# Performance work log

Measured on AMD Instinct MI355X. Metric: run time of the kernel, lower is better.

The kernel has to match this reference:

```python
import jax, jax.numpy as jnp
import numpy as np
from jax import lax

INPUT, HIDDEN, OUT = 5, 32, 2

def setup_inputs() -> dict:
    key = jax.random.key(0)
    ks = jax.random.split(key, 7)
    s_ih = 1.0 / np.sqrt(HIDDEN)
    return {
        "x": jax.random.normal(ks[0], (16384, 200, INPUT), dtype=jnp.float32),
        "W_ih": jax.random.uniform(ks[1], (4 * HIDDEN, INPUT), jnp.float32, -s_ih, s_ih),
        "W_hh": jax.random.uniform(ks[2], (4 * HIDDEN, HIDDEN), jnp.float32, -s_ih, s_ih),
        "b_ih": jax.random.uniform(ks[3], (4 * HIDDEN,), jnp.float32, -s_ih, s_ih),
        "b_hh": jax.random.uniform(ks[4], (4 * HIDDEN,), jnp.float32, -s_ih, s_ih),
        "W_fc": jax.random.uniform(ks[5], (OUT, HIDDEN), jnp.float32, -s_ih, s_ih),
        "b_fc": jax.random.uniform(ks[6], (OUT,), jnp.float32, -s_ih, s_ih),
    }

def reference(x, W_ih, W_hh, b_ih, b_hh, W_fc, b_fc):
    B = x.shape[0]
    # Precompute input projections for all timesteps in one GEMM: [B,T,4H]
    x_proj = jnp.einsum("bti,gi->btg", x, W_ih) + (b_ih + b_hh)
    xs = jnp.swapaxes(x_proj, 0, 1)  # [T, B, 4H]

    def step(carry, xg):
        h, c = carry
        gates = xg + h @ W_hh.T  # [B, 4H]
        i, f, g, o = jnp.split(gates, 4, axis=-1)  # torch gate order i,f,g,o
        i = jax.nn.sigmoid(i)
        f = jax.nn.sigmoid(f)
        g = jnp.tanh(g)
        o = jax.nn.sigmoid(o)
        c = f * c + i * g
        h = o * jnp.tanh(c)
        return (h, c), None

    h0 = jnp.zeros((B, HIDDEN), x.dtype)
    c0 = jnp.zeros((B, HIDDEN), x.dtype)
    (h_n, _), _ = lax.scan(step, (h0, c0), xs)
    return h_n @ W_fc.T + b_fc  # [B, 2]
```

## Files before the change

### kernel.cpp

```cpp
#include <hip/hip_runtime.h>


typedef __bf16 bf16x8 __attribute__((ext_vector_type(8)));
typedef float  f32x4  __attribute__((ext_vector_type(4)));
typedef unsigned int u32;

constexpr int kT = 200, kIN = 5, kH = 32;
constexpr int CT   = 40;
constexpr int HSTR = 40;

union FragU { bf16x8 v; __bf16 b[8]; unsigned short s[8]; u32 u[4]; uint4 q4; };

__device__ __forceinline__ unsigned short bfbits(__bf16 b) {
    union { __bf16 b; unsigned short s; } u; u.b = b; return u.s;
}
__device__ __forceinline__ void split2(float x, __bf16& hi, __bf16& lo) {
    hi = (__bf16)x;
    lo = (__bf16)(x - (float)hi);
}
__device__ __forceinline__ float sigm(float z) {
    return __builtin_amdgcn_rcpf(1.0f + __builtin_amdgcn_exp2f(-1.4426950408889634f * z));
}
__device__ __forceinline__ float tanhv(float z) {
    return fmaf(2.0f,
        __builtin_amdgcn_rcpf(1.0f + __builtin_amdgcn_exp2f(-2.8853900817779268f * z)),
        -1.0f);
}

__global__ __launch_bounds__(128) void lstm_mfma2(
    const float* __restrict__ x,
    const float* __restrict__ W_ih,
    const float* __restrict__ W_hh,
    const float* __restrict__ b_ih,
    const float* __restrict__ b_hh,
    const float* __restrict__ W_fc,
    const float* __restrict__ b_fc,
    float* __restrict__ out)
{
    __shared__ uint4 xbuf[CT][33];
    __shared__ __align__(16) __bf16 hbh[2][16 * HSTR];
    __shared__ __align__(16) __bf16 hbl[2][16 * HSTR];

    const int tid  = threadIdx.x;
    const int wv   = tid >> 6;
    const int lane = tid & 63;
    const int n16  = lane & 15;
    const int q    = lane >> 4;
    const int b0   = blockIdx.x * 16;

    bf16x8 whhh[4], whhl[4], wihf[4];
#pragma unroll
    for (int g = 0; g < 4; ++g) {
        const int t = 2 * g + wv;
        const int r = t * 16 + n16;
        FragU H, L;
#pragma unroll
        for (int j = 0; j < 8; ++j)
            split2(W_hh[r * kH + q * 8 + j], H.b[j], L.b[j]);
        whhh[g] = H.v; whhl[g] = L.v;

        float wr[5];
#pragma unroll
        for (int i = 0; i < 5; ++i) wr[i] = W_ih[r * kIN + i];
        __bf16 bh, bl;
        split2(b_ih[r] + b_hh[r], bh, bl);

        FragU F;
        F.u[0] = F.u[1] = F.u[2] = F.u[3] = 0u;
        if (q == 0) {
#pragma unroll
            for (int i = 0; i < 5; ++i) F.b[i] = (__bf16)wr[i];
#pragma unroll
            for (int i = 0; i < 3; ++i) F.b[5 + i] = (__bf16)wr[i];
        } else if (q == 1) {
            F.b[0] = (__bf16)wr[3];
            F.b[1] = (__bf16)wr[4];
#pragma unroll
            for (int i = 0; i < 5; ++i) {
                __bf16 hb, lb; split2(wr[i], hb, lb);
                F.b[2 + i] = lb;
            }
            F.b[7] = bh;
        } else if (q == 2) {
            F.b[0] = bl;
        }
        wihf[g] = F.v;
    }

    {
        u32* z0 = (u32*)&hbh[0][0];
        u32* z1 = (u32*)&hbl[0][0];
        for (int i = tid; i < (16 * HSTR) / 2; i += 128) { z0[i] = 0u; z1[i] = 0u; }
    }

    float cst[4] = {0.f, 0.f, 0.f, 0.f};

    const int hro = n16 * HSTR + q * 8;
    const int hwo = (q * 4) * HSTR + n16 + 16 * wv;

    auto step = [&](int tc, const __bf16* sh, const __bf16* sl,
                    __bf16* dh, __bf16* dl) {
        FragU xf;
        if (q < 2) {
            xf.q4 = xbuf[tc][n16 * 2 + q];
        } else if (q == 2) {
            xf.u[0] = 0x3F80u; xf.u[1] = 0u; xf.u[2] = 0u; xf.u[3] = 0u;
        } else {
            xf.u[0] = 0u; xf.u[1] = 0u; xf.u[2] = 0u; xf.u[3] = 0u;
        }

        bf16x8 AH = *(const bf16x8*)(sh + hro);
        bf16x8 AL = *(const bf16x8*)(sl + hro);

        f32x4 acc[4];
#pragma unroll
        for (int g = 0; g < 4; ++g) {
            f32x4 a = {0.f, 0.f, 0.f, 0.f};
            a = __builtin_amdgcn_mfma_f32_16x16x32_bf16(xf.v, wihf[g], a, 0, 0, 0);
            a = __builtin_amdgcn_mfma_f32_16x16x32_bf16(AH,   whhh[g], a, 0, 0, 0);
            a = __builtin_amdgcn_mfma_f32_16x16x32_bf16(AH,   whhl[g], a, 0, 0, 0);
            a = __builtin_amdgcn_mfma_f32_16x16x32_bf16(AL,   whhh[g], a, 0, 0, 0);
            acc[g] = a;
        }

#pragma unroll
        for (int r = 0; r < 4; ++r) {
            float iv = sigm (acc[0][r]);
            float fv = sigm (acc[1][r]);
            float gv = tanhv(acc[2][r]);
            float ov = sigm (acc[3][r]);
            float cn = fmaf(fv, cst[r], iv * gv);
            cst[r] = cn;
            float hn = ov * tanhv(cn);
            __bf16 hh, hl;
            split2(hn, hh, hl);
            dh[hwo + r * HSTR] = hh;
            dl[hwo + r * HSTR] = hl;
        }
        __syncthreads();
    };

    for (int phase = 0; phase < kT / CT; ++phase) {
        {
            const int mm = tid >> 3, pp = tid & 7;
            const float* xrow = x + (size_t)(b0 + mm) * (kT * kIN)
                                  + (size_t)(phase * CT + pp * 5) * kIN;
            float xv[25];
#pragma unroll
            for (int i = 0; i < 25; ++i) xv[i] = xrow[i];
#pragma unroll
            for (int s5 = 0; s5 < 5; ++s5) {
                u32 xh[5], xl[5];
#pragma unroll
                for (int i = 0; i < 5; ++i) {
                    __bf16 hb, lb; split2(xv[s5 * 5 + i], hb, lb);
                    xh[i] = bfbits(hb); xl[i] = bfbits(lb);
                }
                uint4 f0 = make_uint4(xh[0] | (xh[1] << 16),
                                      xh[2] | (xh[3] << 16),
                                      xh[4] | (xl[0] << 16),
                                      xl[1] | (xl[2] << 16));
                uint4 f1 = make_uint4(xl[3] | (xl[4] << 16),
                                      xh[0] | (xh[1] << 16),
                                      xh[2] | (xh[3] << 16),
                                      xh[4] | (0x3F80u << 16));
                const int tc = pp * 5 + s5;
                xbuf[tc][mm * 2 + 0] = f0;
                xbuf[tc][mm * 2 + 1] = f1;
            }
        }
        __syncthreads();

#pragma unroll 1
        for (int tc = 0; tc < CT; tc += 2) {
            step(tc,     hbh[0], hbl[0], hbh[1], hbl[1]);
            step(tc + 1, hbh[1], hbl[1], hbh[0], hbl[0]);
        }
    }

    if (tid < 32) {
        const int m = tid >> 1, o = tid & 1;
        float s = b_fc[o];
#pragma unroll
        for (int j = 0; j < kH; ++j) {
            float hv = (float)hbh[0][m * HSTR + j] + (float)hbl[0][m * HSTR + j];
            s = fmaf(hv, W_fc[o * kH + j], s);
        }
        out[(size_t)(b0 + m) * 2 + o] = s;
    }
}

extern "C" void kernel_launch(void* const* d_in, const int* in_sizes, int n_in,
                              void* d_out, int out_size, void* d_ws, size_t ws_size,
                              hipStream_t stream) {
    const float* x    = (const float*)d_in[0];
    const float* W_ih = (const float*)d_in[1];
    const float* W_hh = (const float*)d_in[2];
    const float* b_ih = (const float*)d_in[3];
    const float* b_hh = (const float*)d_in[4];
    const float* W_fc = (const float*)d_in[5];
    const float* b_fc = (const float*)d_in[6];
    float* out = (float*)d_out;

    hipLaunchKernelGGL(lstm_mfma2, dim3(1024), dim3(128), 0, stream,
                       x, W_ih, W_hh, b_ih, b_hh, W_fc, b_fc, out);
}
```

Measured before the change: 283.7 us.

## Keep LSTM hidden state in registers with single-wave transposed MFMA recurrence

Replaces the two-wave block, which exchanged h through shared memory with a barrier every timestep, with a single 64-lane wave. The weights are used as the A operand so each lane's MFMA output rows line up with the B-fragment layout, and h stays in registers across steps. The input projection for the next timestep is issued early as separate MFMAs, overlapping it with the gate math, and the per-step __syncthreads and LDS round trip go away. In exchange each wave now does twice the MFMA and transcendental work, and occupancy halves per block while register pressure rises.

```diff
diff --git a/kernel.cpp b/kernel.cpp
--- a/kernel.cpp
+++ b/kernel.cpp
@@ -6,8 +6,7 @@
 typedef unsigned int u32;
 
 constexpr int kT = 200, kIN = 5, kH = 32;
-constexpr int CT   = 40;
-constexpr int HSTR = 40;
+constexpr int CT = 40;
 
 union FragU { bf16x8 v; __bf16 b[8]; unsigned short s[8]; u32 u[4]; uint4 q4; };
 
@@ -27,7 +26,7 @@
         -1.0f);
 }
 
-__global__ __launch_bounds__(128) void lstm_mfma2(
+__global__ __launch_bounds__(64) void lstm_reg(
     const float* __restrict__ x,
     const float* __restrict__ W_ih,
     const float* __restrict__ W_hh,
@@ -37,33 +36,29 @@
     const float* __restrict__ b_fc,
     float* __restrict__ out)
 {
-    __shared__ uint4 xbuf[CT][33];
-    __shared__ __align__(16) __bf16 hbh[2][16 * HSTR];
-    __shared__ __align__(16) __bf16 hbl[2][16 * HSTR];
-
-    const int tid  = threadIdx.x;
-    const int wv   = tid >> 6;
-    const int lane = tid & 63;
+    __shared__ uint4 xbuf[CT][34];
+
+    const int lane = threadIdx.x;
     const int n16  = lane & 15;
     const int q    = lane >> 4;
     const int b0   = blockIdx.x * 16;
 
-    bf16x8 whhh[4], whhl[4], wihf[4];
-#pragma unroll
-    for (int g = 0; g < 4; ++g) {
-        const int t = 2 * g + wv;
-        const int r = t * 16 + n16;
+    bf16x8 whhA_h[8], whhA_l[8], wihA[8];
+#pragma unroll
+    for (int t8 = 0; t8 < 8; ++t8) {
+        const int g  = t8 & 3, hb = t8 >> 2;
+        const int R  = g * 32 + 8 * (n16 >> 2) + 4 * hb + (n16 & 3);
         FragU H, L;
 #pragma unroll
         for (int j = 0; j < 8; ++j)
-            split2(W_hh[r * kH + q * 8 + j], H.b[j], L.b[j]);
-        whhh[g] = H.v; whhl[g] = L.v;
+            split2(W_hh[R * kH + q * 8 + j], H.b[j], L.b[j]);
+        whhA_h[t8] = H.v; whhA_l[t8] = L.v;
 
         float wr[5];
 #pragma unroll
-        for (int i = 0; i < 5; ++i) wr[i] = W_ih[r * kIN + i];
+        for (int i = 0; i < 5; ++i) wr[i] = W_ih[R * kIN + i];
         __bf16 bh, bl;
-        split2(b_ih[r] + b_hh[r], bh, bl);
+        split2(b_ih[R] + b_hh[R], bh, bl);
 
         FragU F;
         F.u[0] = F.u[1] = F.u[2] = F.u[3] = 0u;
@@ -77,84 +72,50 @@
             F.b[1] = (__bf16)wr[4];
 #pragma unroll
             for (int i = 0; i < 5; ++i) {
-                __bf16 hb, lb; split2(wr[i], hb, lb);
-                F.b[2 + i] = lb;
+                __bf16 hbb, lbb; split2(wr[i], hbb, lbb);
+                F.b[2 + i] = lbb;
             }
             F.b[7] = bh;
         } else if (q == 2) {
             F.b[0] = bl;
         }
-        wihf[g] = F.v;
-    }
-
-    {
-        u32* z0 = (u32*)&hbh[0][0];
-        u32* z1 = (u32*)&hbl[0][0];
-        for (int i = tid; i < (16 * HSTR) / 2; i += 128) { z0[i] = 0u; z1[i] = 0u; }
-    }
-
-    float cst[4] = {0.f, 0.f, 0.f, 0.f};
-
-    const int hro = n16 * HSTR + q * 8;
-    const int hwo = (q * 4) * HSTR + n16 + 16 * wv;
-
-    auto step = [&](int tc, const __bf16* sh, const __bf16* sl,
-                    __bf16* dh, __bf16* dl) {
-        FragU xf;
-        if (q < 2) {
-            xf.q4 = xbuf[tc][n16 * 2 + q];
-        } else if (q == 2) {
-            xf.u[0] = 0x3F80u; xf.u[1] = 0u; xf.u[2] = 0u; xf.u[3] = 0u;
-        } else {
-            xf.u[0] = 0u; xf.u[1] = 0u; xf.u[2] = 0u; xf.u[3] = 0u;
-        }
-
-        bf16x8 AH = *(const bf16x8*)(sh + hro);
-        bf16x8 AL = *(const bf16x8*)(sl + hro);
-
-        f32x4 acc[4];
-#pragma unroll
-        for (int g = 0; g < 4; ++g) {
-            f32x4 a = {0.f, 0.f, 0.f, 0.f};
-            a = __builtin_amdgcn_mfma_f32_16x16x32_bf16(xf.v, wihf[g], a, 0, 0, 0);
-            a = __builtin_amdgcn_mfma_f32_16x16x32_bf16(AH,   whhh[g], a, 0, 0, 0);
-            a = __builtin_amdgcn_mfma_f32_16x16x32_bf16(AH,   whhl[g], a, 0, 0, 0);
-            a = __builtin_amdgcn_mfma_f32_16x16x32_bf16(AL,   whhh[g], a, 0, 0, 0);
-            acc[g] = a;
-        }
-
-#pragma unroll
-        for (int r = 0; r < 4; ++r) {
-            float iv = sigm (acc[0][r]);
-            float fv = sigm (acc[1][r]);
-            float gv = tanhv(acc[2][r]);
-            float ov = sigm (acc[3][r]);
-            float cn = fmaf(fv, cst[r], iv * gv);
-            cst[r] = cn;
-            float hn = ov * tanhv(cn);
-            __bf16 hh, hl;
-            split2(hn, hh, hl);
-            dh[hwo + r * HSTR] = hh;
-            dl[hwo + r * HSTR] = hl;
-        }
-        __syncthreads();
-    };
+        wihA[t8] = F.v;
+    }
+
+    for (int t2 = lane; t2 < CT; t2 += 64) {
+        xbuf[t2][32] = make_uint4(0x3F80u, 0u, 0u, 0u);
+        xbuf[t2][33] = make_uint4(0u, 0u, 0u, 0u);
+    }
+
+    const int col = (q < 2) ? (n16 * 2 + q) : (30 + q);
+    const f32x4 zf4 = {0.f, 0.f, 0.f, 0.f};
+
+    float c8[8] = {0.f, 0.f, 0.f, 0.f, 0.f, 0.f, 0.f, 0.f};
+    float hf[8] = {0.f, 0.f, 0.f, 0.f, 0.f, 0.f, 0.f, 0.f};
+    FragU Bh, Bl;
+    Bh.u[0] = Bh.u[1] = Bh.u[2] = Bh.u[3] = 0u;
+    Bl.u[0] = Bl.u[1] = Bl.u[2] = Bl.u[3] = 0u;
+
+    f32x4 xn[8];
 
     for (int phase = 0; phase < kT / CT; ++phase) {
         {
-            const int mm = tid >> 3, pp = tid & 7;
-            const float* xrow = x + (size_t)(b0 + mm) * (kT * kIN)
-                                  + (size_t)(phase * CT + pp * 5) * kIN;
-            float xv[25];
-#pragma unroll
-            for (int i = 0; i < 25; ++i) xv[i] = xrow[i];
-#pragma unroll
-            for (int s5 = 0; s5 < 5; ++s5) {
+            const int mm = lane >> 2, pp = lane & 3;
+            const float2* xr2 = (const float2*)(x + (size_t)(b0 + mm) * (kT * kIN)
+                                                  + (size_t)(phase * CT + pp * 10) * kIN);
+            float xv[50];
+#pragma unroll
+            for (int i = 0; i < 25; ++i) {
+                float2 v = xr2[i];
+                xv[2 * i] = v.x; xv[2 * i + 1] = v.y;
+            }
+#pragma unroll
+            for (int s5 = 0; s5 < 10; ++s5) {
                 u32 xh[5], xl[5];
 #pragma unroll
                 for (int i = 0; i < 5; ++i) {
-                    __bf16 hb, lb; split2(xv[s5 * 5 + i], hb, lb);
-                    xh[i] = bfbits(hb); xl[i] = bfbits(lb);
+                    __bf16 hbb, lbb; split2(xv[s5 * 5 + i], hbb, lbb);
+                    xh[i] = bfbits(hbb); xl[i] = bfbits(lbb);
                 }
                 uint4 f0 = make_uint4(xh[0] | (xh[1] << 16),
                                       xh[2] | (xh[3] << 16),
@@ -164,28 +125,67 @@
                                       xh[0] | (xh[1] << 16),
                                       xh[2] | (xh[3] << 16),
                                       xh[4] | (0x3F80u << 16));
-                const int tc = pp * 5 + s5;
+                const int tc = pp * 10 + s5;
                 xbuf[tc][mm * 2 + 0] = f0;
                 xbuf[tc][mm * 2 + 1] = f1;
             }
         }
         __syncthreads();
 
+        {
+            FragU xg; xg.q4 = xbuf[0][col];
+#pragma unroll
+            for (int t8 = 0; t8 < 8; ++t8)
+                xn[t8] = __builtin_amdgcn_mfma_f32_16x16x32_bf16(wihA[t8], xg.v, zf4, 0, 0, 0);
+        }
+
 #pragma unroll 1
-        for (int tc = 0; tc < CT; tc += 2) {
-            step(tc,     hbh[0], hbl[0], hbh[1], hbl[1]);
-            step(tc + 1, hbh[1], hbl[1], hbh[0], hbl[0]);
-        }
-    }
-
-    if (tid < 32) {
-        const int m = tid >> 1, o = tid & 1;
+        for (int tc = 0; tc < CT; ++tc) {
+            f32x4 acc[8];
+#pragma unroll
+            for (int t8 = 0; t8 < 8; ++t8) {
+                f32x4 a = __builtin_amdgcn_mfma_f32_16x16x32_bf16(whhA_h[t8], Bh.v, xn[t8], 0, 0, 0);
+                a = __builtin_amdgcn_mfma_f32_16x16x32_bf16(whhA_h[t8], Bl.v, a, 0, 0, 0);
+                a = __builtin_amdgcn_mfma_f32_16x16x32_bf16(whhA_l[t8], Bh.v, a, 0, 0, 0);
+                acc[t8] = a;
+            }
+
+            {
+                const int tn = (tc + 1 < CT) ? tc + 1 : 0;
+                FragU xg; xg.q4 = xbuf[tn][col];
+#pragma unroll
+                for (int t8 = 0; t8 < 8; ++t8)
+                    xn[t8] = __builtin_amdgcn_mfma_f32_16x16x32_bf16(wihA[t8], xg.v, zf4, 0, 0, 0);
+            }
+
+#pragma unroll
+            for (int jj = 0; jj < 8; ++jj) {
+                const int hb = jj >> 2, r = jj & 3;
+                float iv = sigm (acc[hb * 4 + 0][r]);
+                float fv = sigm (acc[hb * 4 + 1][r]);
+                float gv = tanhv(acc[hb * 4 + 2][r]);
+                float ov = sigm (acc[hb * 4 + 3][r]);
+                float cn = fmaf(fv, c8[jj], iv * gv);
+                c8[jj] = cn;
+                float hn = ov * tanhv(cn);
+                hf[jj] = hn;
+                split2(hn, Bh.b[jj], Bl.b[jj]);
+            }
+        }
+    }
+
+    float* hfin = (float*)xbuf;
+    __syncthreads();
+#pragma unroll
+    for (int jj = 0; jj < 8; ++jj)
+        hfin[n16 * 33 + q * 8 + jj] = hf[jj];
+    __syncthreads();
+    if (lane < 32) {
+        const int m = lane >> 1, o = lane & 1;
         float s = b_fc[o];
 #pragma unroll
-        for (int j = 0; j < kH; ++j) {
-            float hv = (float)hbh[0][m * HSTR + j] + (float)hbl[0][m * HSTR + j];
-            s = fmaf(hv, W_fc[o * kH + j], s);
-        }
+        for (int j = 0; j < kH; ++j)
+            s = fmaf(hfin[m * 33 + j], W_fc[o * kH + j], s);
         out[(size_t)(b0 + m) * 2 + o] = s;
     }
 }
@@ -202,6 +202,6 @@
     const float* b_fc = (const float*)d_in[6];
     float* out = (float*)d_out;
 
-    hipLaunchKernelGGL(lstm_mfma2, dim3(1024), dim3(128), 0, stream,
+    hipLaunchKernelGGL(lstm_reg, dim3(1024), dim3(64), 0, stream,
                        x, W_ih, W_hh, b_ih, b_hh, W_fc, b_fc, out);
 }
```

Result: faster. 275.1 us (-3.0%).
